# Kernel optimization log

Measured on AMD Instinct MI355X. Metric: run time of the kernel, lower is better.

## Reference

```python
import jax, jax.numpy as jnp
import numpy as np

N = 50000
F_IN = 512
H1 = 500
H2 = 100
C = 16
E = 800000


def setup_inputs() -> dict:
    key = jax.random.key(0)
    ks = jax.random.split(key, 8)
    x = jax.random.normal(ks[0], (N, F_IN), dtype=jnp.float32)
    edge_index = jax.random.randint(ks[1], (2, E), 0, N, dtype=jnp.int64)
    W1 = jax.random.normal(ks[2], (F_IN, H1), dtype=jnp.float32) / np.sqrt(F_IN)
    b1 = jnp.zeros((H1,), dtype=jnp.float32)
    W2 = jax.random.normal(ks[3], (H1, H2), dtype=jnp.float32) / np.sqrt(H1)
    b2 = jnp.zeros((H2,), dtype=jnp.float32)
    W3 = jax.random.normal(ks[4], (H2, C), dtype=jnp.float32) / np.sqrt(H2)
    b3 = jnp.zeros((C,), dtype=jnp.float32)
    return {"x": x, "edge_index": edge_index, "W1": W1, "b1": b1,
            "W2": W2, "b2": b2, "W3": W3, "b3": b3}


def _edge_norm(edge_index, num_nodes):
    # add self loops (as in torch add_self_loops), then symmetric degree norm
    loops = jnp.arange(num_nodes, dtype=edge_index.dtype)
    row = jnp.concatenate([edge_index[0], loops])
    col = jnp.concatenate([edge_index[1], loops])
    deg = jax.ops.segment_sum(jnp.ones_like(row, dtype=jnp.float32), row,
                              num_segments=num_nodes)
    dinv = jnp.where(deg > 0, deg ** -0.5, 0.0)  # norm[isinf] = 0
    norm = dinv[row] * dinv[col]
    return row, col, norm


def _graph_conv(x, row, col, norm, W, b, num_nodes):
    h = x @ W + b                                  # [N, out]
    msg = norm[:, None] * h[col]                   # gather + scale, [E', out]
    return jax.ops.segment_sum(msg, row, num_segments=num_nodes)  # SpMM


def reference(x, edge_index, W1, b1, W2, b2, W3, b3):
    num_nodes = x.shape[0]
    row, col, norm = _edge_norm(edge_index, num_nodes)
    h = jnp.tanh(_graph_conv(x, row, col, norm, W1, b1, num_nodes))
    h = jnp.tanh(_graph_conv(h, row, col, norm, W2, b2, num_nodes))
    h = jnp.tanh(_graph_conv(h, row, col, norm, W3, b3, num_nodes))
    return jax.nn.softmax(h, axis=1)
```

## Files before the change

kernel.cpp:

```cpp
#include <hip/hip_runtime.h>
#include <math.h>

#define NN  50000
#define FIN 512
#define HH1 500
#define HH2 100
#define NC  16
#define NE  800000
#define KD  512

typedef __attribute__((ext_vector_type(4))) float    f32x4;
typedef __attribute__((ext_vector_type(4))) _Float16 f16x4;
typedef __attribute__((ext_vector_type(8))) _Float16 f16x8;
typedef __attribute__((ext_vector_type(8))) unsigned short u16x8;
typedef __attribute__((ext_vector_type(4))) unsigned short u16x4;


__global__ void zero2_k(int* a, int* b) {
    int i = blockIdx.x * blockDim.x + threadIdx.x;
    if (i < NN) { a[i] = 0; b[i] = 0; }
}

__global__ void hist_k(const int* __restrict__ rows, int* __restrict__ rowcnt) {
    int i = blockIdx.x * blockDim.x + threadIdx.x;
    if (i < NE) atomicAdd(&rowcnt[rows[i]], 1);
}

__global__ void dinv_k(const int* __restrict__ rowcnt, float* __restrict__ dinv) {
    int i = blockIdx.x * blockDim.x + threadIdx.x;
    if (i < NN) dinv[i] = rsqrtf((float)(rowcnt[i] + 1));
}

__global__ __launch_bounds__(1024) void scan1_k(const int* __restrict__ cnt,
                                                int* __restrict__ excl,
                                                int* __restrict__ bsum) {
    __shared__ int s[1024];
    int t = threadIdx.x;
    int i = blockIdx.x * 1024 + t;
    int v = (i < NN) ? cnt[i] : 0;
    s[t] = v;
    __syncthreads();
    #pragma unroll
    for (int off = 1; off < 1024; off <<= 1) {
        int add = (t >= off) ? s[t - off] : 0;
        __syncthreads();
        s[t] += add;
        __syncthreads();
    }
    if (i < NN) excl[i] = s[t] - v;
    if (t == 1023) bsum[blockIdx.x] = s[1023];
}

__global__ void scan2_k(int* bsum, int nb) {
    int lane = threadIdx.x;
    int orig = (lane < nb) ? bsum[lane] : 0;
    int v = orig;
    #pragma unroll
    for (int off = 1; off < 64; off <<= 1) {
        int u = __shfl_up(v, off, 64);
        if (lane >= off) v += u;
    }
    if (lane < nb) bsum[lane] = v - orig;
}

__global__ void scan3_k(const int* __restrict__ excl, const int* __restrict__ bsum,
                        int* __restrict__ ptr) {
    int i = blockIdx.x * 256 + threadIdx.x;
    if (i < NN) ptr[i] = excl[i] + bsum[i >> 10];
}

__global__ void scatter_k(const int* __restrict__ rows, const int* __restrict__ cols,
                          const float* __restrict__ dinv,
                          const int* __restrict__ row_ptr, int* __restrict__ fill,
                          int2* __restrict__ cw) {
    int e = blockIdx.x * blockDim.x + threadIdx.x;
    if (e >= NE) return;
    int r = rows[e], c = cols[e];
    int pos = row_ptr[r] + atomicAdd(&fill[r], 1);
    cw[pos] = make_int2(c, __float_as_int(dinv[r] * dinv[c]));
}


#define R1 (512 * 512)
#define R2 (128 * 512)
#define R3 (128 * 128)

__global__ void wconv3_k(const float* __restrict__ W1, const float* __restrict__ W2,
                         const float* __restrict__ W3, _Float16* __restrict__ Wt1,
                         _Float16* __restrict__ Wt2, _Float16* __restrict__ Wt3)
{
    int idx = blockIdx.x * 256 + threadIdx.x;
    if (idx < R1) {
        int n_ = idx >> 9, kk = idx & 511;
        float v = (n_ < HH1) ? W1[(size_t)kk * HH1 + n_] : 0.0f;
        Wt1[idx] = (_Float16)v;
    } else if (idx < R1 + R2) {
        int j = idx - R1;
        int n_ = j >> 9, kk = j & 511;
        float v = (kk < HH1 && n_ < HH2) ? W2[(size_t)kk * HH2 + n_] : 0.0f;
        Wt2[j] = (_Float16)v;
    } else if (idx < R1 + R2 + R3) {
        int j = idx - R1 - R2;
        int n_ = j >> 7, kk = j & 127;
        float v = (kk < HH2 && n_ < NC) ? W3[(size_t)kk * NC + n_] : 0.0f;
        Wt3[j] = (_Float16)v;
    }
}


__global__ __launch_bounds__(256) void cvtx_k(const float4* __restrict__ x,
                                              f16x8* __restrict__ xh) {
    int i = blockIdx.x * 256 + threadIdx.x;
    float4 v0 = x[2 * i], v1 = x[2 * i + 1];
    f16x8 h = {(_Float16)v0.x, (_Float16)v0.y, (_Float16)v0.z, (_Float16)v0.w,
               (_Float16)v1.x, (_Float16)v1.y, (_Float16)v1.z, (_Float16)v1.w};
    __builtin_nontemporal_store(h, xh + i);
}


typedef unsigned int u32g;

__device__ __forceinline__ void g2l16(const void* g, void* l) {
    __builtin_amdgcn_global_load_lds(
        (const __attribute__((address_space(1))) u32g*)g,
        (__attribute__((address_space(3))) u32g*)l, 16, 0, 0);
}

template<int BCOLS, int COUT, int KK>
__global__ __launch_bounds__(256, 3) void gemm_lds_k(
    const _Float16* __restrict__ A,
    const _Float16* __restrict__ Wt,
    const float* __restrict__ bias, _Float16* __restrict__ Cb,
    int mpad, int n, int m)
{
    constexpr int NBF   = BCOLS / 64;
    constexpr int WC    = BCOLS / 4;
    constexpr int NSTEP = KK / 32;

    __shared__ __align__(16) _Float16 As[2][64 * 32];
    __shared__ __align__(16) _Float16 Bs[2][BCOLS * 32];

    int tid  = threadIdx.x;
    int lane = tid & 63;
    int w    = tid >> 6;
    int lr = lane & 15, q = lane >> 4;
    int row0 = blockIdx.x * 64;
    int col0 = blockIdx.y * BCOLS;

    f32x4 acc[4][NBF];
    #pragma unroll
    for (int i = 0; i < 4; i++)
        #pragma unroll
        for (int j = 0; j < NBF; j++) acc[i][j] = (f32x4){0.f, 0.f, 0.f, 0.f};

    auto stage = [&](int kt, int bf) {
        {
            int rr = tid >> 2, c8 = tid & 3;
            int c8s = c8 ^ ((rr >> 1) & 3);
            int gr = row0 + rr; if (gr >= n) gr = n - 1;
            g2l16(A + (size_t)gr * KK + kt + c8s * 8, &As[bf][tid * 8]);
        }
        #pragma unroll
        for (int i = 0; i < NBF; i++) {
            int idx = i * 256 + tid;
            int rr = idx >> 2, c8 = idx & 3;
            int c8s = c8 ^ ((rr >> 1) & 3);
            g2l16(Wt + (size_t)(col0 + rr) * KK + kt + c8s * 8, &Bs[bf][idx * 8]);
        }
    };

    stage(0, 0);
    int bf = 0;
    #pragma unroll
    for (int step = 0; step < NSTEP; step++) {
        __syncthreads();
        if (step + 1 < NSTEP) stage((step + 1) * 32, bf ^ 1);

        f16x8 a[4], b[NBF];
        #pragma unroll
        for (int t = 0; t < 4; t++) {
            int row = t * 16 + lr;
            a[t] = *(const f16x8*)&As[bf][(row * 4 + (q ^ ((row >> 1) & 3))) * 8];
        }
        #pragma unroll
        for (int t = 0; t < NBF; t++) {
            int row = w * WC + t * 16 + lr;
            b[t] = *(const f16x8*)&Bs[bf][(row * 4 + (q ^ ((row >> 1) & 3))) * 8];
        }
        #pragma unroll
        for (int ti = 0; ti < 4; ti++)
            #pragma unroll
            for (int tj = 0; tj < NBF; tj++)
                acc[ti][tj] = __builtin_amdgcn_mfma_f32_16x16x32_f16(
                    a[ti], b[tj], acc[ti][tj], 0, 0, 0);
        bf ^= 1;
    }

    #pragma unroll
    for (int ti = 0; ti < 4; ti++) {
        #pragma unroll
        for (int tj = 0; tj < NBF; tj++) {
            int col = col0 + w * WC + tj * 16 + lr;
            if (COUT == 0 && col >= mpad) continue;
            bool valid = col < m;
            float bv = valid ? bias[col] : 0.0f;
            #pragma unroll
            for (int p = 0; p < 4; p++) {
                int row = row0 + ti * 16 + q * 4 + p;
                if (row < n) {
                    float v = valid ? (acc[ti][tj][p] + bv) : 0.0f;
                    if (COUT == 1) {
                        size_t addr = (size_t)(col >> 8) * ((size_t)NN * 256)
                                    + (size_t)row * 256 + (col & 255);
                        Cb[addr] = (_Float16)v;
                    } else {
                        Cb[(size_t)row * mpad + col] = (_Float16)v;
                    }
                }
            }
        }
    }
}


__device__ __forceinline__ void fma_mix8(float* acc, u16x8 v, float w) {
    union { u16x8 u; unsigned int d[4]; } t; t.u = v;
    #pragma unroll
    for (int k = 0; k < 4; k++) {
        asm("v_fma_mix_f32 %0, %1, %2, %0 op_sel:[0,0,0] op_sel_hi:[1,0,0]"
            : "+v"(acc[2 * k]) : "v"(t.d[k]), "v"(w));
        asm("v_fma_mix_f32 %0, %1, %2, %0 op_sel:[1,0,0] op_sel_hi:[1,0,0]"
            : "+v"(acc[2 * k + 1]) : "v"(t.d[k]), "v"(w));
    }
}

__device__ __forceinline__ void fma_mix4(float* acc, u16x4 v, float w) {
    union { u16x4 u; unsigned int d[2]; } t; t.u = v;
    #pragma unroll
    for (int k = 0; k < 2; k++) {
        asm("v_fma_mix_f32 %0, %1, %2, %0 op_sel:[0,0,0] op_sel_hi:[1,0,0]"
            : "+v"(acc[2 * k]) : "v"(t.d[k]), "v"(w));
        asm("v_fma_mix_f32 %0, %1, %2, %0 op_sel:[1,0,0] op_sel_hi:[1,0,0]"
            : "+v"(acc[2 * k + 1]) : "v"(t.d[k]), "v"(w));
    }
}


__global__ __launch_bounds__(256) void spmm_f16_256_k(
    const int* __restrict__ row_ptr, const int* __restrict__ rowcnt,
    const int2* __restrict__ cw, const float* __restrict__ dinv,
    const _Float16* __restrict__ hc,
    _Float16* __restrict__ outh, int fbase)
{
    int r = blockIdx.x * 4 + (threadIdx.x >> 6);
    int lane = threadIdx.x & 63;
    if (r >= NN) return;

    const u16x4* h4 = (const u16x4*)hc;

    float acc[4];
    #pragma unroll
    for (int i = 0; i < 4; i++) acc[i] = 0.f;

    float d = dinv[r];
    fma_mix4(acc, h4[(size_t)r * 64 + lane], d * d);

    int beg = row_ptr[r], cnt = rowcnt[r];
    for (int base = 0; base < cnt; base += 64) {
        int m = (cnt - base < 64) ? (cnt - base) : 64;
        int2 vc = (lane < m) ? cw[beg + base + lane] : make_int2(0, 0);
        int P = (m + 7) & ~7;
        for (int j = 0; j < P; j += 8) {
            u16x4 vv[8]; float wl[8];
            #pragma unroll
            for (int u = 0; u < 8; u++) {
                int c  = __builtin_amdgcn_readlane(vc.x, j + u);
                int wb = __builtin_amdgcn_readlane(vc.y, j + u);
                wl[u] = __int_as_float(wb);
                vv[u] = h4[(size_t)c * 64 + lane];
            }
            #pragma unroll
            for (int u = 0; u < 8; u++) fma_mix4(acc, vv[u], wl[u]);
        }
    }

    int f0 = fbase + lane * 4;
    f16x4 o;
    #pragma unroll
    for (int i = 0; i < 4; i++)
        o[i] = (_Float16)((f0 + i < HH1) ? tanhf(acc[i]) : 0.0f);
    __builtin_nontemporal_store(o, (f16x4*)(outh + (size_t)r * KD + f0));
}


__global__ __launch_bounds__(256) void spmm_f16_100_k(
    const int* __restrict__ row_ptr, const int* __restrict__ rowcnt,
    const int2* __restrict__ cw, const float* __restrict__ dinv,
    const _Float16* __restrict__ hb, _Float16* __restrict__ outh)
{
    int r = blockIdx.x * 16 + (threadIdx.x >> 4);
    int lane = threadIdx.x & 15;
    if (r >= NN) return;

    const u16x8* h8 = (const u16x8*)hb;

    float acc[8];
    #pragma unroll
    for (int i = 0; i < 8; i++) acc[i] = 0.f;

    float d = dinv[r];
    fma_mix8(acc, h8[(size_t)r * 16 + lane], d * d);

    int beg = row_ptr[r], cnt = rowcnt[r];
    int j = 0;
    for (; j + 7 < cnt; j += 8) {
        int2  e[8];
        u16x8 v[8];
        #pragma unroll
        for (int u = 0; u < 8; u++) e[u] = cw[beg + j + u];
        #pragma unroll
        for (int u = 0; u < 8; u++) v[u] = h8[(size_t)e[u].x * 16 + lane];
        #pragma unroll
        for (int u = 0; u < 8; u++) fma_mix8(acc, v[u], __int_as_float(e[u].y));
    }
    for (; j < cnt; j++) {
        int2 e = cw[beg + j];
        fma_mix8(acc, h8[(size_t)e.x * 16 + lane], __int_as_float(e.y));
    }

    int f0 = lane * 8;
    f16x8 o;
    #pragma unroll
    for (int i = 0; i < 8; i++)
        o[i] = (_Float16)((f0 + i < HH2) ? tanhf(acc[i]) : 0.0f);
    __builtin_nontemporal_store(o, (f16x8*)(outh + (size_t)r * 128 + f0));
}


__global__ __launch_bounds__(256) void spmm3h_k(
    const int* __restrict__ row_ptr, const int* __restrict__ rowcnt,
    const int2* __restrict__ cw, const float* __restrict__ dinv,
    const _Float16* __restrict__ hb, float* __restrict__ out)
{
    int r = blockIdx.x * 128 + (threadIdx.x >> 1);
    int lane = threadIdx.x & 1;
    if (r >= NN) return;

    const u16x8* h8 = (const u16x8*)hb;

    float acc[8];
    #pragma unroll
    for (int i = 0; i < 8; i++) acc[i] = 0.f;

    float d = dinv[r];
    fma_mix8(acc, h8[(size_t)r * 2 + lane], d * d);

    int beg = row_ptr[r], cnt = rowcnt[r];
    int j = 0;
    for (; j + 3 < cnt; j += 4) {
        int2  e0 = cw[beg + j],     e1 = cw[beg + j + 1];
        int2  e2 = cw[beg + j + 2], e3 = cw[beg + j + 3];
        u16x8 v0 = h8[(size_t)e0.x * 2 + lane];
        u16x8 v1 = h8[(size_t)e1.x * 2 + lane];
        u16x8 v2 = h8[(size_t)e2.x * 2 + lane];
        u16x8 v3 = h8[(size_t)e3.x * 2 + lane];
        fma_mix8(acc, v0, __int_as_float(e0.y));
        fma_mix8(acc, v1, __int_as_float(e1.y));
        fma_mix8(acc, v2, __int_as_float(e2.y));
        fma_mix8(acc, v3, __int_as_float(e3.y));
    }
    for (; j < cnt; j++) {
        int2 e = cw[beg + j];
        fma_mix8(acc, h8[(size_t)e.x * 2 + lane], __int_as_float(e.y));
    }

    float* o = out + (size_t)r * NC + lane * 8;
    f32x4 a0 = {acc[0], acc[1], acc[2], acc[3]};
    f32x4 a1 = {acc[4], acc[5], acc[6], acc[7]};
    __builtin_nontemporal_store(a0, (f32x4*)o);
    __builtin_nontemporal_store(a1, (f32x4*)(o + 4));
}

__global__ void tanh_softmax_k(const float* __restrict__ in, float* __restrict__ out) {
    int r = blockIdx.x * blockDim.x + threadIdx.x;
    if (r >= NN) return;
    float v[NC];
    float mx = -1e30f;
    #pragma unroll
    for (int j = 0; j < NC; j++) {
        v[j] = tanhf(in[r * NC + j]);
        mx = fmaxf(mx, v[j]);
    }
    float s = 0.0f;
    #pragma unroll
    for (int j = 0; j < NC; j++) { v[j] = expf(v[j] - mx); s += v[j]; }
    float inv = 1.0f / s;
    #pragma unroll
    for (int j = 0; j < NC; j++) out[r * NC + j] = v[j] * inv;
}


extern "C" void kernel_launch(void* const* d_in, const int* in_sizes, int n_in,
                              void* d_out, int out_size, void* d_ws, size_t ws_size,
                              hipStream_t stream)
{
    const float* x  = (const float*)d_in[0];
    const int*   ei = (const int*)d_in[1];
    const float* W1 = (const float*)d_in[2];
    const float* b1 = (const float*)d_in[3];
    const float* W2 = (const float*)d_in[4];
    const float* b2 = (const float*)d_in[5];
    const float* W3 = (const float*)d_in[6];
    const float* b3 = (const float*)d_in[7];
    float* out = (float*)d_out;

    const int* rows = ei;
    const int* cols = ei + NE;

    char* p = (char*)d_ws;
    float*     dinv    = (float*)p;     p += (size_t)NN * 4;
    int*       rowcnt  = (int*)p;       p += (size_t)NN * 4;
    int*       row_ptr = (int*)p;       p += (size_t)NN * 4;
    int*       fill    = (int*)p;       p += (size_t)NN * 4;
    int*       excl    = (int*)p;       p += (size_t)NN * 4;
    int*       bsum    = (int*)p;       p += (size_t)256 * 4;
    int2*      cw      = (int2*)p;      p += (size_t)NE * 8;
    float*     B3      = (float*)p;     p += (size_t)NN * NC * 4;
    _Float16*  A1h     = (_Float16*)p;  p += (size_t)NN * KD * 2;
    _Float16*  h1h     = (_Float16*)p;  p += (size_t)NN * KD * 2;
    _Float16*  A2h     = (_Float16*)p;  p += (size_t)NN * 128 * 2;
    _Float16*  h2h     = (_Float16*)p;  p += (size_t)NN * 128 * 2;
    _Float16*  A3h     = (_Float16*)p;  p += (size_t)NN * NC * 2;
    _Float16*  Wt1     = (_Float16*)p;  p += (size_t)R1 * 2;
    _Float16*  Wt2     = (_Float16*)p;  p += (size_t)R2 * 2;
    _Float16*  Wt3     = (_Float16*)p;  p += (size_t)R3 * 2;

    _Float16* xh = h1h;

    const int T = 256;
    const int NB = (NN + 1023) / 1024;
    const int GB = (NN + 63) / 64;

    wconv3_k<<<(R1 + R2 + R3) / 256, T, 0, stream>>>(W1, W2, W3, Wt1, Wt2, Wt3);
    cvtx_k<<<(NN * FIN / 8) / 256, T, 0, stream>>>((const float4*)x, (f16x8*)xh);
    zero2_k<<<(NN + T - 1) / T, T, 0, stream>>>(rowcnt, fill);
    hist_k<<<(NE + T - 1) / T, T, 0, stream>>>(rows, rowcnt);
    dinv_k<<<(NN + T - 1) / T, T, 0, stream>>>(rowcnt, dinv);
    scan1_k<<<NB, 1024, 0, stream>>>(rowcnt, excl, bsum);
    scan2_k<<<1, 64, 0, stream>>>(bsum, NB);
    scan3_k<<<(NN + T - 1) / T, T, 0, stream>>>(excl, bsum, row_ptr);
    scatter_k<<<(NE + T - 1) / T, T, 0, stream>>>(rows, cols, dinv, row_ptr, fill, cw);

    {
        gemm_lds_k<256, 1, 512><<<dim3(GB, 2), T, 0, stream>>>(
            xh, Wt1, b1, A1h, KD, NN, HH1);
        spmm_f16_256_k<<<(NN + 3) / 4, T, 0, stream>>>(row_ptr, rowcnt, cw, dinv,
                                                       A1h, h1h, 0);
        spmm_f16_256_k<<<(NN + 3) / 4, T, 0, stream>>>(row_ptr, rowcnt, cw, dinv,
                                                       A1h + (size_t)NN * 256, h1h, 256);
    }
    {
        gemm_lds_k<128, 0, 512><<<dim3(GB, 1), T, 0, stream>>>(
            h1h, Wt2, b2, A2h, 128, NN, HH2);
        spmm_f16_100_k<<<(NN + 15) / 16, T, 0, stream>>>(row_ptr, rowcnt, cw,
                                                         dinv, A2h, h2h);
    }
    {
        gemm_lds_k<64, 0, 128><<<dim3(GB, 1), T, 0, stream>>>(
            h2h, Wt3, b3, A3h, NC, NN, NC);
        spmm3h_k<<<(NN + 127) / 128, T, 0, stream>>>(row_ptr, rowcnt, cw,
                                                     dinv, A3h, B3);
        tanh_softmax_k<<<(NN + T - 1) / T, T, 0, stream>>>(B3, out);
    }
}
```

Before: 546.6 us.

## Fuse fp32-to-fp16 input conversion into first-layer GEMM with full-width tiles

Removes the separate pass that converts x to fp16. The new first-layer GEMM loads fp32 rows of x into registers, converts them and stores them into swizzled LDS while weights stream in through global_load_lds. Each block now covers all 512 output columns, so A is read once instead of twice. This saves writing and re-reading a 51 MB fp16 copy, at the cost of larger LDS use, more accumulator registers and lower occupancy (launch bounds 256,2).

```diff
diff --git a/kernel.cpp b/kernel.cpp
--- a/kernel.cpp
+++ b/kernel.cpp
@@ -108,16 +108,6 @@
 }
 
 
-__global__ __launch_bounds__(256) void cvtx_k(const float4* __restrict__ x,
-                                              f16x8* __restrict__ xh) {
-    int i = blockIdx.x * 256 + threadIdx.x;
-    float4 v0 = x[2 * i], v1 = x[2 * i + 1];
-    f16x8 h = {(_Float16)v0.x, (_Float16)v0.y, (_Float16)v0.z, (_Float16)v0.w,
-               (_Float16)v1.x, (_Float16)v1.y, (_Float16)v1.z, (_Float16)v1.w};
-    __builtin_nontemporal_store(h, xh + i);
-}
-
-
 typedef unsigned int u32g;
 
 __device__ __forceinline__ void g2l16(const void* g, void* l) {
@@ -125,6 +115,110 @@
         (const __attribute__((address_space(1))) u32g*)g,
         (__attribute__((address_space(3))) u32g*)l, 16, 0, 0);
 }
+
+
+__global__ __launch_bounds__(256, 2) void gemm1_k(
+    const float* __restrict__ A, const _Float16* __restrict__ Wt,
+    const float* __restrict__ bias, _Float16* __restrict__ Cb, int n)
+{
+    __shared__ __align__(16) _Float16 As[2][64 * 32];
+    __shared__ __align__(16) _Float16 Bs[2][512 * 32];
+
+    int tid  = threadIdx.x;
+    int lane = tid & 63;
+    int w    = tid >> 6;
+    int lr = lane & 15, q = lane >> 4;
+    int row0 = blockIdx.x * 64;
+
+    f32x4 acc[4][8];
+    #pragma unroll
+    for (int i = 0; i < 4; i++)
+        #pragma unroll
+        for (int j = 0; j < 8; j++) acc[i][j] = (f32x4){0.f, 0.f, 0.f, 0.f};
+
+    int arr = tid >> 2, ac8 = tid & 3;
+    int ac8s = ac8 ^ ((arr >> 1) & 3);
+    int gr = row0 + arr; if (gr >= n) gr = n - 1;
+    const float* asrc = A + (size_t)gr * 512 + ac8s * 8;
+
+    float4 pav[2][2];
+
+    auto aload = [&](int kt, int par) {
+        pav[par][0] = *(const float4*)(asrc + kt);
+        pav[par][1] = *(const float4*)(asrc + kt + 4);
+    };
+    auto astore = [&](int bf, int par) {
+        float4 v0 = pav[par][0], v1 = pav[par][1];
+        f16x8 h = {(_Float16)v0.x, (_Float16)v0.y, (_Float16)v0.z, (_Float16)v0.w,
+                   (_Float16)v1.x, (_Float16)v1.y, (_Float16)v1.z, (_Float16)v1.w};
+        *(f16x8*)&As[bf][tid * 8] = h;
+    };
+    auto bstage = [&](int kt, int bf) {
+        #pragma unroll
+        for (int i = 0; i < 8; i++) {
+            int id = i * 256 + tid;
+            int rr = id >> 2, c8 = id & 3;
+            int c8s = c8 ^ ((rr >> 1) & 3);
+            g2l16(Wt + (size_t)rr * 512 + kt + c8s * 8, &Bs[bf][id * 8]);
+        }
+    };
+
+    aload(0, 0);
+    aload(32, 1);
+    bstage(0, 0);
+    astore(0, 0);
+    __syncthreads();
+
+    #pragma unroll
+    for (int step = 0; step < 16; step++) {
+        int bf = step & 1;
+        int par = step & 1;
+        if (step + 2 < 16) aload((step + 2) * 32, par);
+        if (step + 1 < 16) bstage((step + 1) * 32, bf ^ 1);
+
+        f16x8 a[4], b[8];
+        #pragma unroll
+        for (int t = 0; t < 4; t++) {
+            int row = t * 16 + lr;
+            a[t] = *(const f16x8*)&As[bf][(row * 4 + (q ^ ((row >> 1) & 3))) * 8];
+        }
+        #pragma unroll
+        for (int t = 0; t < 8; t++) {
+            int row = w * 128 + t * 16 + lr;
+            b[t] = *(const f16x8*)&Bs[bf][(row * 4 + (q ^ ((row >> 1) & 3))) * 8];
+        }
+        #pragma unroll
+        for (int ti = 0; ti < 4; ti++)
+            #pragma unroll
+            for (int tj = 0; tj < 8; tj++)
+                acc[ti][tj] = __builtin_amdgcn_mfma_f32_16x16x32_f16(
+                    a[ti], b[tj], acc[ti][tj], 0, 0, 0);
+
+        if (step + 1 < 16) astore(bf ^ 1, par ^ 1);
+        __syncthreads();
+        (void)bf;
+    }
+
+    #pragma unroll
+    for (int ti = 0; ti < 4; ti++) {
+        #pragma unroll
+        for (int tj = 0; tj < 8; tj++) {
+            int col = w * 128 + tj * 16 + lr;
+            bool valid = col < HH1;
+            float bv = valid ? bias[col] : 0.0f;
+            size_t cbase = (size_t)(col >> 8) * ((size_t)NN * 256) + (col & 255);
+            #pragma unroll
+            for (int p = 0; p < 4; p++) {
+                int row = row0 + ti * 16 + q * 4 + p;
+                if (row < n) {
+                    float v = valid ? (acc[ti][tj][p] + bv) : 0.0f;
+                    Cb[cbase + (size_t)row * 256] = (_Float16)v;
+                }
+            }
+        }
+    }
+}
+
 
 template<int BCOLS, int COUT, int KK>
 __global__ __launch_bounds__(256, 3) void gemm_lds_k(
@@ -435,14 +529,11 @@
     _Float16*  Wt2     = (_Float16*)p;  p += (size_t)R2 * 2;
     _Float16*  Wt3     = (_Float16*)p;  p += (size_t)R3 * 2;
 
-    _Float16* xh = h1h;
-
     const int T = 256;
     const int NB = (NN + 1023) / 1024;
     const int GB = (NN + 63) / 64;
 
     wconv3_k<<<(R1 + R2 + R3) / 256, T, 0, stream>>>(W1, W2, W3, Wt1, Wt2, Wt3);
-    cvtx_k<<<(NN * FIN / 8) / 256, T, 0, stream>>>((const float4*)x, (f16x8*)xh);
     zero2_k<<<(NN + T - 1) / T, T, 0, stream>>>(rowcnt, fill);
     hist_k<<<(NE + T - 1) / T, T, 0, stream>>>(rows, rowcnt);
     dinv_k<<<(NN + T - 1) / T, T, 0, stream>>>(rowcnt, dinv);
@@ -452,8 +543,7 @@
     scatter_k<<<(NE + T - 1) / T, T, 0, stream>>>(rows, cols, dinv, row_ptr, fill, cw);
 
     {
-        gemm_lds_k<256, 1, 512><<<dim3(GB, 2), T, 0, stream>>>(
-            xh, Wt1, b1, A1h, KD, NN, HH1);
+        gemm1_k<<<GB, T, 0, stream>>>(x, Wt1, b1, A1h, NN);
         spmm_f16_256_k<<<(NN + 3) / 4, T, 0, stream>>>(row_ptr, rowcnt, cw, dinv,
                                                        A1h, h1h, 0);
         spmm_f16_256_k<<<(NN + 3) / 4, T, 0, stream>>>(row_ptr, rowcnt, cw, dinv,
```

Result: no change. 547.1 us (+0.1%).
